# Performance work log

Hardware: AMD Instinct MI355X
Metric: run time of the kernel (lower is better)

Reference implementation:

```python
import jax, jax.numpy as jnp
import numpy as np

K = 16          # patch_size
P2 = 256        # patch_size**2
D_PD = 512      # learned base dictionary atoms (D_out_lam_pd)
D_LAM = 112     # adaptive atoms from sdict, = 8*14 (D_out_lam)
DD = D_PD + D_LAM  # 624
T = 5
INDICE = 112
MIN_V, MAX_V = 0.0, 1.0


def _idx(H, W, k, stride):
    oh = (H - k) // stride + 1
    ow = (W - k) // stride + 1
    r = jnp.arange(k)[:, None] + stride * jnp.arange(oh)[None, :]  # [k, oh]
    c = jnp.arange(k)[:, None] + stride * jnp.arange(ow)[None, :]  # [k, ow]
    return r[:, None, :, None], c[None, :, None, :], oh, ow


def _unfold(x, k, stride):
    # torch.nn.Unfold: [N, C*k*k, L] with (C, kh, kw) channel order, row-major L
    N, C, H, W = x.shape
    r, c, oh, ow = _idx(H, W, k, stride)
    return x[:, :, r, c].reshape(N, C * k * k, oh * ow)


def _fold(p, H, W, k):
    # torch.nn.functional.fold (col2im) with stride 1, overlap-add
    N, ckk, L = p.shape
    r, c, oh, ow = _idx(H, W, k, 1)
    C = ckk // (k * k)
    out = jnp.zeros((N, C, H, W), p.dtype)
    return out.at[:, :, r, c].add(p.reshape(N, C, k, k, oh, ow))


def _mlp(x, ws):
    # Linear + clamp(min=0) chain, no relu after last layer (dropout = eval identity)
    for w, b in ws[:-1]:
        x = jnp.maximum(x @ w + b, 0.0)
    w, b = ws[-1]
    return x @ w + b


def _cbam(x, w1, w2, conv_w):
    # standard CBAM: channel attention (shared MLP on avg+max pool) then 7x7 spatial attention
    def mlp(v):
        return jnp.maximum(v @ w1, 0.0) @ w2
    ca = jax.nn.sigmoid(mlp(x.mean(axis=(2, 3))) + mlp(x.max(axis=(2, 3))))
    x = x * ca[:, :, None, None]
    s = jnp.stack([x.mean(axis=1), x.max(axis=1)], axis=1)  # [N,2,h,w]
    sa = jax.lax.conv_general_dilated(s, conv_w, (1, 1), [(3, 3), (3, 3)],
                                      dimension_numbers=('NCHW', 'OIHW', 'NCHW'))
    return x * jax.nn.sigmoid(sa)


def _soft(x, l):
    return jnp.sign(x) * jnp.maximum(jnp.abs(x) - l, 0.0)


def _stage(img, Dict, c, sd_ws, ca1, ca2, saw, lam_ws, pd_ws, w_ws):
    N, C, H, W = img.shape
    uf = _unfold(img, K, 1).transpose(0, 2, 1)     # [N, L, 256]
    uf1 = _unfold(img, K, 8).transpose(0, 2, 1)    # [N, L1, 256]
    step = uf1.shape[1] // INDICE                  # static under jit
    ext = uf1[:, ::step, :][:, :INDICE, :]         # [N, 112, 256]
    sd = _mlp(ext, sd_ws)                          # linears1..4
    sd = sd / jnp.maximum(jnp.linalg.norm(sd, axis=-1, keepdims=True), 1e-12)
    sd = _cbam(sd.transpose(0, 2, 1).reshape(N, P2, 8, 14), ca1, ca2, saw)
    sd = sd.reshape(N, P2, INDICE)                 # [N, 256, 112]
    Dcat = jnp.concatenate([jnp.broadcast_to(Dict, (N,) + Dict.shape), sd], axis=-1)  # [N,256,624]
    # thresholds: l = cat(lpd, ls)
    thr = jnp.concatenate([_mlp(uf, pd_ws) / c, _mlp(uf, lam_ws) / c], axis=-1)  # [N,L,624]
    y = uf @ Dcat                                  # [N, L, 624]
    # S = (I - D^T D / c)^T; D^T D is symmetric so the transpose is a no-op
    S = jnp.eye(DD, dtype=img.dtype) - (Dcat.transpose(0, 2, 1) @ Dcat) / c
    z = _soft(y, thr)
    for _ in range(T):  # LISTA unrolled iterations (T static)
        z = _soft(z @ S + y / c, thr)
    Wg = jax.nn.sigmoid(_mlp(uf, w_ws))            # [N, L, 256]
    x_pred = jnp.clip(z @ Dcat.transpose(0, 2, 1), MIN_V, MAX_V) * Wg
    num = _fold(x_pred.transpose(0, 2, 1), H, W, K)
    den = _fold(Wg.transpose(0, 2, 1), H, W, K)    # fold of W * ones
    return num / den


def _forward(x, Dict, c, s1w, s1b, s2w, s2b, s3w, s3b, s4w, s4b, caw1, caw2, saw,
             a1w, a1b, a2w, a2b, a3w, a3b, p1w, p1b, p2w, p2b, p3w, p3b,
             b1w, b1b, b2w, b2b, b3w, b3b, q1w, q1b, q2w, q2b, q3w, q3b,
             w1w, w1b, w2w, w2b, w3w, w3b):
    sd_ws = [(s1w, s1b), (s2w, s2b), (s3w, s3b), (s4w, s4b)]
    w_ws = [(w1w, w1b), (w2w, w2b), (w3w, w3b)]
    res = _stage(x, Dict, c, sd_ws, caw1, caw2, saw,
                 [(a1w, a1b), (a2w, a2b), (a3w, a3b)],
                 [(p1w, p1b), (p2w, p2b), (p3w, p3b)], w_ws)
    res = _stage(res, Dict, c, sd_ws, caw1, caw2, saw,
                 [(b1w, b1b), (b2w, b2b), (b3w, b3b)],
                 [(q1w, q1b), (q2w, q2b), (q3w, q3b)], w_ws)
    return res


def setup_inputs() -> dict:
    key = jax.random.key(0)
    ks = iter(jax.random.split(key, 40))
    d = {}
    d['x'] = jax.random.uniform(next(ks), (2, 1, 128, 128), jnp.float32)
    Dm = jax.random.normal(next(ks), (P2, D_PD), jnp.float32)
    d['Dict'] = Dm / jnp.linalg.norm(Dm, axis=0, keepdims=True)  # unit-norm atoms
    d['c'] = jnp.asarray(10.0, jnp.float32)  # c > ||D^T D||_2
    dims = {'s1': (256, 512), 's2': (512, 1024), 's3': (1024, 512), 's4': (512, 256),
            'a1': (256, 1024), 'a2': (1024, 512), 'a3': (512, 112),
            'p1': (256, 1024), 'p2': (1024, 512), 'p3': (512, 512),
            'b1': (256, 1024), 'b2': (1024, 512), 'b3': (512, 112),
            'q1': (256, 1024), 'q2': (1024, 512), 'q3': (512, 512),
            'w1': (256, 1024), 'w2': (1024, 512), 'w3': (512, 256)}
    for name, (i, o) in dims.items():
        d[name + 'w'] = jax.random.normal(next(ks), (i, o), jnp.float32) / np.float32(np.sqrt(i))
        d[name + 'b'] = jnp.zeros((o,), jnp.float32)
    d['caw1'] = jax.random.normal(next(ks), (256, 512), jnp.float32) / np.float32(16.0)
    d['caw2'] = jax.random.normal(next(ks), (512, 256), jnp.float32) / np.float32(np.sqrt(512))
    d['saw'] = jax.random.normal(next(ks), (1, 2, 7, 7), jnp.float32) * np.float32(0.1)
    return d


def reference(x, Dict, c, s1w, s1b, s2w, s2b, s3w, s3b, s4w, s4b, caw1, caw2, saw,
              a1w, a1b, a2w, a2b, a3w, a3b, p1w, p1b, p2w, p2b, p3w, p3b,
              b1w, b1b, b2w, b2b, b3w, b3b, q1w, q1b, q2w, q2b, q3w, q3b,
              w1w, w1b, w2w, w2b, w3w, w3b):
    return _forward(x, Dict, c, s1w, s1b, s2w, s2b, s3w, s3b, s4w, s4b, caw1, caw2, saw,
                    a1w, a1b, a2w, a2b, a3w, a3b, p1w, p1b, p2w, p2b, p3w, p3b,
                    b1w, b1b, b2w, b2b, b3w, b3b, q1w, q1b, q2w, q2b, q3w, q3b,
                    w1w, w1b, w2w, w2b, w3w, w3b)
```

## Files before the change

### kernel.cpp

```cpp
#include <hip/hip_runtime.h>
#include <hip/hip_bf16.h>
#include <math.h>

#define L_LOC 12769
#define NB 2
#define NLR (NB * L_LOC)
#define NW 19

typedef short short8v __attribute__((ext_vector_type(8)));
typedef float f32x4 __attribute__((ext_vector_type(4)));
typedef __hip_bfloat16 bf16;

__device__ __forceinline__ float softf(float x, float l) {
  float a = fmaxf(fabsf(x) - l, 0.0f);
  return x > 0.0f ? a : (x < 0.0f ? -a : 0.0f);
}
__device__ __forceinline__ float sigf(float x) { return 1.0f / (1.0f + expf(-x)); }
__device__ __forceinline__ void split2(float v, bf16& h, bf16& l) {
  h = __float2bfloat16(v);
  l = __float2bfloat16(v - __bfloat162float(h));
}

enum { ME_RELU = 0, ME_SCALE = 1, ME_SIG = 2, ME_Y = 3, ME_SOFT = 4, ME_XP = 5,
       ME_SMAT = 6, ME_LIN = 7 };

template <int EPI, int TERMS, int WLO>
__global__ __launch_bounds__(256) void mgemm_k(
    const bf16* __restrict__ A, int lda, size_t aOff,
    const bf16* __restrict__ B0, const bf16* __restrict__ B1, int ldb, size_t bOff,
    void* __restrict__ Cv, int ldc, size_t cOff,
    bf16* __restrict__ Zp,
    const float* __restrict__ bias,
    const float* __restrict__ E1, const float* __restrict__ E2, int lde,
    const float* __restrict__ cptr, int bRow, int Rc, int r0, int N, int K)
{
  const int NPA = (TERMS >= 3) ? 2 : 1;
  const int NPB = (TERMS >= 2) ? 2 : 1;
  __shared__ char As[(TERMS >= 3) ? 2 : 1][8192];
  __shared__ char Bs[(TERMS >= 2) ? 2 : 1][8192];
  const int t = threadIdx.x;
  const int lane = t & 63, wv = t >> 6;
  const int wr = wv >> 1, wc = wv & 1;
  const int m0 = blockIdx.x * 128, n0 = blockIdx.y * 128;
  const int nb = (m0 >= bRow) ? 1 : 0;
  const bf16* __restrict__ Bt = nb ? B1 : B0;
  const int row16 = lane & 15, kg = lane >> 4;
  const int grow = t >> 2;
  const int gcol = (t & 3) * 8;
  f32x4 acc[4][4];
#pragma unroll
  for (int i = 0; i < 4; ++i)
#pragma unroll
    for (int j = 0; j < 4; ++j) { acc[i][j][0] = 0.f; acc[i][j][1] = 0.f; acc[i][j][2] = 0.f; acc[i][j][3] = 0.f; }

  for (int k0 = 0; k0 < K; k0 += 32) {
#pragma unroll
    for (int h = 0; h < NPA; ++h)
#pragma unroll
      for (int i = 0; i < 2; ++i) {
        const bf16* ga = A + h * aOff + (size_t)(m0 + i * 64 + grow) * lda + k0 + gcol;
        __builtin_amdgcn_global_load_lds(
            (const __attribute__((address_space(1))) void*)ga,
            (__attribute__((address_space(3))) void*)(As[h] + i * 4096 + wv * 1024), 16, 0, 0);
      }
#pragma unroll
    for (int h = 0; h < NPB; ++h)
#pragma unroll
      for (int i = 0; i < 2; ++i) {
        const bf16* gb = Bt + h * bOff + (size_t)(n0 + i * 64 + grow) * ldb + k0 + gcol;
        __builtin_amdgcn_global_load_lds(
            (const __attribute__((address_space(1))) void*)gb,
            (__attribute__((address_space(3))) void*)(Bs[h] + i * 4096 + wv * 1024), 16, 0, 0);
      }
    __syncthreads();
    short8v ah[4], al[4], bh[4], bl[4];
#pragma unroll
    for (int mi = 0; mi < 4; ++mi) {
      int o = (wr * 64 + mi * 16 + row16) * 64 + kg * 16;
      ah[mi] = *(const short8v*)(As[0] + o);
      if (TERMS >= 3) al[mi] = *(const short8v*)(As[NPA - 1] + o);
    }
#pragma unroll
    for (int ni = 0; ni < 4; ++ni) {
      int o = (wc * 64 + ni * 16 + row16) * 64 + kg * 16;
      bh[ni] = *(const short8v*)(Bs[0] + o);
      if (TERMS >= 2) bl[ni] = *(const short8v*)(Bs[NPB - 1] + o);
    }
#pragma unroll
    for (int mi = 0; mi < 4; ++mi)
#pragma unroll
      for (int ni = 0; ni < 4; ++ni) {
        if (TERMS >= 2)
          acc[mi][ni] = __builtin_amdgcn_mfma_f32_16x16x32_bf16(ah[mi], bl[ni], acc[mi][ni], 0, 0, 0);
        if (TERMS >= 3)
          acc[mi][ni] = __builtin_amdgcn_mfma_f32_16x16x32_bf16(al[mi], bh[ni], acc[mi][ni], 0, 0, 0);
        acc[mi][ni] = __builtin_amdgcn_mfma_f32_16x16x32_bf16(ah[mi], bh[ni], acc[mi][ni], 0, 0, 0);
      }
    __syncthreads();
  }

  float invc = 1.0f;
  if (EPI == ME_SCALE || EPI == ME_SOFT || EPI == ME_SMAT) invc = 1.0f / cptr[0];
  bf16* Cb = (bf16*)Cv;
  float* Cf = (float*)Cv;
#pragma unroll
  for (int ni = 0; ni < 4; ++ni) {
    int col = n0 + wc * 64 + ni * 16 + row16;
    const bool colok = col < N;
    float bv = 0.0f;
    if ((EPI == ME_RELU || EPI == ME_SCALE || EPI == ME_SIG || EPI == ME_LIN) && colok)
      bv = bias[col];
#pragma unroll
    for (int mi = 0; mi < 4; ++mi) {
      int rowb = m0 + wr * 64 + mi * 16 + kg * 4;
#pragma unroll
      for (int r = 0; r < 4; ++r) {
        int row = rowb + r;
        float v = acc[mi][ni][r];
        if (EPI == ME_RELU) {
          if (colok) {
            float o = fmaxf(v + bv, 0.0f);
            size_t ci = (size_t)row * ldc + col;
            if (WLO) {
              bf16 h, l; split2(o, h, l);
              Cb[ci] = h; Cb[ci + cOff] = l;
            } else {
              Cb[ci] = __float2bfloat16(o);
            }
          }
        } else if (EPI == ME_LIN) {
          if (colok && row < Rc) Cf[(size_t)row * ldc + col] = v + bv;
        } else if (EPI == ME_SCALE) {
          if (colok) Cf[(size_t)row * ldc + col] = (v + bv) * invc;
        } else if (EPI == ME_SIG) {
          if (colok) {
            int rl = row - nb * bRow;
            if (rl < Rc && rl >= 0)
              Cf[(size_t)col * NLR + (size_t)nb * L_LOC + r0 + rl] = sigf(v + bv);
          }
        } else if (EPI == ME_Y) {
          if (colok) {
            size_t e = (size_t)row * lde + col;
            Cf[(size_t)row * ldc + col] = v;
            Zp[(size_t)row * 640 + col] = __float2bfloat16(softf(v, E1[e]));
          }
        } else if (EPI == ME_SOFT) {
          if (colok) {
            size_t e = (size_t)row * lde + col;
            Cb[(size_t)row * ldc + col] = __float2bfloat16(softf(v + E1[e] * invc, E2[e]));
          }
        } else if (EPI == ME_XP) {
          int rl = row - nb * bRow;
          if (colok && rl < Rc && rl >= 0) {
            size_t g = (size_t)col * NLR + (size_t)nb * L_LOC + r0 + rl;
            Cf[g] = fminf(fmaxf(v, 0.0f), 1.0f) * E1[g];
          }
        } else {
          float o = (row < 624 && col < 624) ? ((row == col ? 1.0f : 0.0f) - v * invc) : 0.0f;
          bf16 h, l; split2(o, h, l);
          size_t ci = (size_t)row * ldc + col;
          Cb[ci] = h; Cb[ci + cOff] = l;
        }
      }
    }
  }
}

static void mgemm(hipStream_t st, int EPI, int terms, int wlo,
                  const bf16* A, int lda, size_t aOff,
                  const bf16* B0, const bf16* B1, int ldb, size_t bOff,
                  void* C, int ldc, size_t cOff,
                  bf16* Zp,
                  const float* bias, const float* E1, const float* E2, int lde,
                  const float* cptr, int bRow, int Rc, int r0,
                  int Mp, int N, int K)
{
  dim3 grid(Mp / 128, (N + 127) / 128), blk(256);
#define MG(ep, tm, wl) mgemm_k<ep, tm, wl><<<grid, blk, 0, st>>>(A, lda, aOff, B0, B1, ldb, bOff, C, ldc, cOff, Zp, bias, E1, E2, lde, cptr, bRow, Rc, r0, N, K)
  if (EPI == ME_RELU && terms == 1 && !wlo) { MG(ME_RELU, 1, 0); }
  else if (EPI == ME_RELU && terms == 1)    { MG(ME_RELU, 1, 1); }
  else if (EPI == ME_RELU)                  { MG(ME_RELU, 3, 1); }
  else if (EPI == ME_LIN)                   { MG(ME_LIN, 3, 0); }
  else if (EPI == ME_SCALE)                 { MG(ME_SCALE, 3, 0); }
  else if (EPI == ME_SIG)                   { MG(ME_SIG, 1, 0); }
  else if (EPI == ME_Y)                     { MG(ME_Y, 3, 0); }
  else if (EPI == ME_SOFT)                  { MG(ME_SOFT, 2, 0); }
  else if (EPI == ME_XP)                    { MG(ME_XP, 2, 0); }
  else                                      { MG(ME_SMAT, 3, 0); }
#undef MG
}

struct WTable {
  const float* src[NW];
  bf16* dst[NW];
  int K[NW], N[NW], Kp[NW], Np[NW];
  long long loOff[NW];
  int base[NW + 1];
};

__global__ void wtransall_k(WTable w) {
  int idx = blockIdx.x * 256 + threadIdx.x;
  if (idx >= w.base[NW]) return;
  int s = 0;
  while (s < NW - 1 && idx >= w.base[s + 1]) ++s;
  int li = idx - w.base[s];
  int Kp = w.Kp[s];
  int n = li / Kp, k = li - n * Kp;
  float v = (n < w.N[s] && k < w.K[s]) ? w.src[s][(size_t)k * w.N[s] + n] : 0.0f;
  bf16 h, l; split2(v, h, l);
  w.dst[s][li] = h;
  w.dst[s][li + w.loOff[s]] = l;
}

__global__ void extb_k(const float* __restrict__ img, bf16* __restrict__ dst) {
  int idx = blockIdx.x * 256 + threadIdx.x;
  int row = idx >> 8, p = idx & 255;
  float v = 0.0f;
  if (row < 224) {
    int n = row / 112, e = row - n * 112;
    int l1 = 2 * e, i1 = l1 / 15, j1 = l1 - i1 * 15;
    v = img[n * 16384 + (8 * i1 + (p >> 4)) * 128 + 8 * j1 + (p & 15)];
  }
  bf16 h, l; split2(v, h, l);
  dst[idx] = h; dst[idx + 65536] = l;
}

__global__ void rownorm224_k(float* sd) {
  int r = blockIdx.x, t = threadIdx.x;
  float v[4], s = 0.0f;
#pragma unroll
  for (int j = 0; j < 4; ++j) { v[j] = sd[r * 256 + t + 64 * j]; s += v[j] * v[j]; }
#pragma unroll
  for (int o = 1; o < 64; o <<= 1) s += __shfl_xor(s, o);
  float sc = 1.0f / fmaxf(sqrtf(s), 1e-12f);
#pragma unroll
  for (int j = 0; j < 4; ++j) sd[r * 256 + t + 64 * j] = v[j] * sc;
}

__global__ void meanmax_k(const float* __restrict__ sd, float* mv, float* xv) {
  int id = blockIdx.x * 256 + threadIdx.x;
  int n = id >> 8, ch = id & 255;
  float s = 0.0f, m = -INFINITY;
  for (int e = 0; e < 112; ++e) {
    float v = sd[(n * 112 + e) * 256 + ch];
    s += v; m = fmaxf(m, v);
  }
  mv[id] = s * (1.0f / 112.0f);
  xv[id] = m;
}

__global__ void cah_k(const float* __restrict__ mv, const float* __restrict__ xv,
                      const float* __restrict__ w1, float* hm, float* hx) {
  int id = blockIdx.x * 256 + threadIdx.x;
  int n = id >> 9, o = id & 511;
  float sm = 0.0f, sx = 0.0f;
#pragma unroll 4
  for (int i = 0; i < 256; ++i) {
    float w = w1[i * 512 + o];
    sm = fmaf(mv[n * 256 + i], w, sm);
    sx = fmaf(xv[n * 256 + i], w, sx);
  }
  hm[id] = fmaxf(sm, 0.0f);
  hx[id] = fmaxf(sx, 0.0f);
}

__global__ void cao_k(const float* __restrict__ hm, const float* __restrict__ hx,
                      const float* __restrict__ w2, float* ca) {
  int id = blockIdx.x * 256 + threadIdx.x;
  int n = id >> 8, ch = id & 255;
  float s = 0.0f;
#pragma unroll 4
  for (int o = 0; o < 512; ++o)
    s = fmaf(hm[n * 512 + o] + hx[n * 512 + o], w2[o * 256 + ch], s);
  ca[id] = sigf(s);
}

__global__ void spatial_k(const float* __restrict__ sd, const float* __restrict__ ca,
                          const float* __restrict__ saw, float* __restrict__ Dcat) {
  __shared__ float smean[112], smax[112];
  const int n = blockIdx.x, t = threadIdx.x;
  if (t < 112) {
    float sum = 0.0f, mx = -INFINITY;
    for (int ch = 0; ch < 256; ++ch) {
      float v = sd[(n * 112 + t) * 256 + ch] * ca[n * 256 + ch];
      Dcat[(size_t)n * 159744 + ch * 624 + 512 + t] = v;
      sum += v; mx = fmaxf(mx, v);
    }
    smean[t] = sum * (1.0f / 256.0f);
    smax[t] = mx;
  }
  __syncthreads();
  if (t < 112) {
    int h = t / 14, w = t % 14;
    float acc = 0.0f;
    for (int dh = 0; dh < 7; ++dh) {
      int hh = h + dh - 3; if (hh < 0 || hh >= 8) continue;
      for (int dw = 0; dw < 7; ++dw) {
        int ww = w + dw - 3; if (ww < 0 || ww >= 14) continue;
        int sp = hh * 14 + ww;
        acc += smean[sp] * saw[dh * 7 + dw] + smax[sp] * saw[49 + dh * 7 + dw];
      }
    }
    float sg = sigf(acc);
    for (int ch = 0; ch < 256; ++ch) Dcat[(size_t)n * 159744 + ch * 624 + 512 + t] *= sg;
  }
}

__global__ void dcatconv_k(const float* __restrict__ Dict, const float* __restrict__ Dc,
                           bf16* __restrict__ Db, bf16* __restrict__ DbT) {
  int idx = blockIdx.x * 256 + threadIdx.x;
  if (idx >= 327680) return;
  int n = idx / 163840, r = idx - n * 163840;
  int p = r / 640, a = r - p * 640;
  float v = 0.0f;
  if (a < 512)      v = Dict[p * 512 + a];
  else if (a < 624) v = Dc[(size_t)n * 159744 + p * 624 + a];
  bf16 h, l; split2(v, h, l);
  size_t base = (size_t)n * 327680;
  Db[base + p * 640 + a] = h;
  Db[base + 163840 + p * 640 + a] = l;
  DbT[base + (size_t)a * 256 + p] = h;
  DbT[base + 163840 + (size_t)a * 256 + p] = l;
}

__global__ void unfold_k(const float* __restrict__ img, bf16* __restrict__ uf,
                         int r0, int Rc, int bRowc, size_t pOff) {
  int bi = blockIdx.x;
  int nb = bi >= Rc;
  int rl = nb ? bi - Rc : bi;
  int row = nb * bRowc + rl;
  int p = threadIdx.x;
  int l = r0 + rl;
  int i0 = l / 113, j0 = l - i0 * 113;
  float v = img[nb * 16384 + (i0 + (p >> 4)) * 128 + j0 + (p & 15)];
  bf16 h, lo; split2(v, h, lo);
  size_t o = (size_t)row * 256 + p;
  uf[o] = h; uf[o + pOff] = lo;
}

__global__ void folddiv_k(const float* __restrict__ xpT, const float* __restrict__ wgT,
                          float* __restrict__ out) {
  int idx = blockIdx.x * 256 + threadIdx.x;
  if (idx >= 32768) return;
  int n = idx >> 14, rem = idx & 16383;
  int i = rem >> 7, j = rem & 127;
  float num = 0.0f, den = 0.0f;
  int kh0 = (i - 112 > 0) ? i - 112 : 0;
  int kh1 = (i < 15) ? i : 15;
  int kw0 = (j - 112 > 0) ? j - 112 : 0;
  int kw1 = (j < 15) ? j : 15;
  for (int kh = kh0; kh <= kh1; ++kh)
    for (int kw = kw0; kw <= kw1; ++kw) {
      int l = (i - kh) * 113 + (j - kw);
      size_t base = (size_t)(kh * 16 + kw) * NLR + (size_t)n * L_LOC + l;
      num += xpT[base];
      den += wgT[base];
    }
  out[idx] = num / den;
}

struct Bufs {
  float *xp, *wg, *Dcat_f, *sd, *res;
  float *mv, *xv, *hm, *hx, *ca;
  bf16 *Db, *DbT, *Sb;
  bf16 *extb, *sdh1, *sdh2, *sdh3;
  bf16 *uf, *h1, *h2, *z, *zn;
  float *thr, *y;
  size_t ufO, h2O;
  int R;
};

static void run_stage(hipStream_t st, const float* const* in, const float* img,
                      float* outimg, int pd0, int lam0,
                      bf16* const* WtPd, bf16* const* WtLam, bf16* const* WtW,
                      bf16* const* Ws, const Bufs& b)
{
  const float* cptr = in[2];
  const int BIG = 1 << 30;
  extb_k<<<dim3(256), dim3(256), 0, st>>>(img, b.extb);
  mgemm(st, ME_RELU, 3, 1, b.extb, 256, 65536, Ws[0], Ws[0], 256, 512 * 256,
        b.sdh1, 512, 256 * 512, 0, in[4], 0, 0, 0, cptr, BIG, 224, 0, 256, 512, 256);
  mgemm(st, ME_RELU, 3, 1, b.sdh1, 512, 256 * 512, Ws[1], Ws[1], 512, 1024 * 512,
        b.sdh2, 1024, 256 * 1024, 0, in[6], 0, 0, 0, cptr, BIG, 224, 0, 256, 1024, 512);
  mgemm(st, ME_RELU, 3, 1, b.sdh2, 1024, 256 * 1024, Ws[2], Ws[2], 1024, 512 * 1024,
        b.sdh3, 512, 256 * 512, 0, in[8], 0, 0, 0, cptr, BIG, 224, 0, 256, 512, 1024);
  mgemm(st, ME_LIN, 3, 0, b.sdh3, 512, 256 * 512, Ws[3], Ws[3], 512, 256 * 512,
        b.sd, 256, 0, 0, in[10], 0, 0, 0, cptr, BIG, 224, 0, 256, 256, 512);
  rownorm224_k<<<dim3(224), dim3(64), 0, st>>>(b.sd);
  meanmax_k<<<dim3(2), dim3(256), 0, st>>>(b.sd, b.mv, b.xv);
  cah_k<<<dim3(4), dim3(256), 0, st>>>(b.mv, b.xv, in[41], b.hm, b.hx);
  cao_k<<<dim3(2), dim3(256), 0, st>>>(b.hm, b.hx, in[42], b.ca);
  spatial_k<<<dim3(2), dim3(128), 0, st>>>(b.sd, b.ca, in[43], b.Dcat_f);
  dcatconv_k<<<dim3(1280), dim3(256), 0, st>>>(in[1], b.Dcat_f, b.Db, b.DbT);
  for (int n = 0; n < NB; ++n) {
    const bf16* Dt = b.DbT + (size_t)n * 327680;
    mgemm(st, ME_SMAT, 3, 0, Dt, 256, 163840, Dt, Dt, 256, 163840,
          b.Sb + (size_t)n * 819200, 640, 409600, 0,
          0, 0, 0, 0, cptr, BIG, 624, 0, 640, 640, 256);
  }

  for (int r0 = 0; r0 < L_LOC; r0 += b.R) {
    int Rc = L_LOC - r0; if (Rc > b.R) Rc = b.R;
    int bRowc = ((Rc + 127) / 128) * 128;
    int Mp = 2 * bRowc;
    unfold_k<<<dim3(2 * Rc), dim3(256), 0, st>>>(img, b.uf, r0, Rc, bRowc, b.ufO);
    mgemm(st, ME_RELU, 1, 0, b.uf, 256, b.ufO, WtPd[0], WtPd[0], 256, 1024 * 256,
          b.h1, 1024, 0, 0, in[pd0 + 1], 0, 0, 0, cptr, bRowc, Rc, r0, Mp, 1024, 256);
    mgemm(st, ME_RELU, 1, 1, b.h1, 1024, 0, WtPd[1], WtPd[1], 1024, 512 * 1024,
          b.h2, 512, b.h2O, 0, in[pd0 + 3], 0, 0, 0, cptr, bRowc, Rc, r0, Mp, 512, 1024);
    mgemm(st, ME_SCALE, 3, 0, b.h2, 512, b.h2O, WtPd[2], WtPd[2], 512, 512 * 512,
          b.thr, 640, 0, 0, in[pd0 + 5], 0, 0, 0, cptr, bRowc, Rc, r0, Mp, 512, 512);
    mgemm(st, ME_RELU, 1, 0, b.uf, 256, b.ufO, WtLam[0], WtLam[0], 256, 1024 * 256,
          b.h1, 1024, 0, 0, in[lam0 + 1], 0, 0, 0, cptr, bRowc, Rc, r0, Mp, 1024, 256);
    mgemm(st, ME_RELU, 1, 1, b.h1, 1024, 0, WtLam[1], WtLam[1], 1024, 512 * 1024,
          b.h2, 512, b.h2O, 0, in[lam0 + 3], 0, 0, 0, cptr, bRowc, Rc, r0, Mp, 512, 1024);
    mgemm(st, ME_SCALE, 3, 0, b.h2, 512, b.h2O, WtLam[2], WtLam[2], 512, 128 * 512,
          b.thr + 512, 640, 0, 0, in[lam0 + 5], 0, 0, 0, cptr, bRowc, Rc, r0, Mp, 112, 512);
    mgemm(st, ME_RELU, 1, 0, b.uf, 256, b.ufO, WtW[0], WtW[0], 256, 1024 * 256,
          b.h1, 1024, 0, 0, in[36], 0, 0, 0, cptr, bRowc, Rc, r0, Mp, 1024, 256);
    mgemm(st, ME_RELU, 1, 1, b.h1, 1024, 0, WtW[1], WtW[1], 1024, 512 * 1024,
          b.h2, 512, b.h2O, 0, in[38], 0, 0, 0, cptr, bRowc, Rc, r0, Mp, 512, 1024);
    mgemm(st, ME_SIG, 1, 0, b.h2, 512, b.h2O, WtW[2], WtW[2], 512, 256 * 512,
          b.wg, 0, 0, 0, in[40], 0, 0, 0, cptr, bRowc, Rc, r0, Mp, 256, 512);
    mgemm(st, ME_Y, 3, 0, b.uf, 256, b.ufO, b.DbT, b.DbT + 327680, 256, 163840,
          b.y, 640, 0, b.z, 0, b.thr, 0, 640, cptr, bRowc, Rc, r0, Mp, 624, 256);
    bf16* zi = b.z; bf16* zo = b.zn;
    for (int it = 0; it < 5; ++it) {
      mgemm(st, ME_SOFT, 2, 0, zi, 640, 0, b.Sb, b.Sb + 819200, 640, 409600,
            zo, 640, 0, 0, 0, b.y, b.thr, 640, cptr, bRowc, Rc, r0, Mp, 624, 640);
      bf16* tmp = zi; zi = zo; zo = tmp;
    }
    mgemm(st, ME_XP, 2, 0, zi, 640, 0, b.Db, b.Db + 327680, 640, 163840,
          b.xp, 0, 0, 0, 0, b.wg, 0, 0, cptr, bRowc, Rc, r0, Mp, 256, 640);
  }
  folddiv_k<<<dim3(128), dim3(256), 0, st>>>(b.xp, b.wg, outimg);
}

extern "C" void kernel_launch(void* const* d_in, const int* in_sizes, int n_in,
                              void* d_out, int out_size, void* d_ws, size_t ws_size,
                              hipStream_t stream)
{
  (void)in_sizes; (void)n_in; (void)out_size;
  const float* const* in = (const float* const*)d_in;
  char* base = (char*)d_ws;
  size_t off = 0;
  auto allocf = [&](size_t nelem) -> float* {
    float* p = (float*)(base + off);
    off += ((nelem * 4 + 255) / 256) * 256;
    return p;
  };
  auto allocb2 = [&](size_t nelem) -> bf16* {
    bf16* p = (bf16*)(base + off);
    off += ((nelem * 2 * 2 + 255) / 256) * 256;
    return p;
  };
  auto allocb1 = [&](size_t nelem) -> bf16* {
    bf16* p = (bf16*)(base + off);
    off += ((nelem * 2 + 255) / 256) * 256;
    return p;
  };
  Bufs b;
  b.xp = allocf((size_t)NLR * 256);
  b.wg = allocf((size_t)NLR * 256);
  b.Dcat_f = allocf(2 * 256 * 624);
  b.sd = allocf(224 * 256);
  b.res = allocf(2 * 16384);
  b.mv = allocf(512); b.xv = allocf(512);
  b.hm = allocf(1024); b.hx = allocf(1024);
  b.ca = allocf(512);
  b.Db = allocb2(2 * 163840);
  b.DbT = allocb2(2 * 163840);
  b.Sb = allocb2(2 * 409600);
  b.extb = allocb2(256 * 256);
  b.sdh1 = allocb2(256 * 512);
  b.sdh2 = allocb2(256 * 1024);
  b.sdh3 = allocb2(256 * 512);

  bf16 *Wa[3], *Wp[3], *Wb[3], *Wq[3], *Ww[3], *Ws[4];
  WTable wt;
  int ne = 0, tot = 0;
  auto addw = [&](const float* src, bf16* dst, int K, int N, int Kp, int Np) {
    wt.src[ne] = src; wt.dst[ne] = dst;
    wt.K[ne] = K; wt.N[ne] = N; wt.Kp[ne] = Kp; wt.Np[ne] = Np;
    wt.loOff[ne] = (long long)Np * Kp; wt.base[ne] = tot;
    tot += Np * Kp; ++ne;
  };
  int sdK[4] = {256, 512, 1024, 512}, sdN[4] = {512, 1024, 512, 256}, sdIdx[4] = {3, 5, 7, 9};
  for (int i = 0; i < 4; ++i) {
    Ws[i] = allocb2((size_t)sdN[i] * sdK[i]);
    addw(in[sdIdx[i]], Ws[i], sdK[i], sdN[i], sdK[i], sdN[i]);
  }
  struct WD { bf16** slot; int idx, K, N, Kp, Np; };
  WD wd[15] = {
    {&Wa[0], 11, 256, 1024, 256, 1024}, {&Wa[1], 13, 1024, 512, 1024, 512}, {&Wa[2], 15, 512, 112, 512, 128},
    {&Wp[0], 17, 256, 1024, 256, 1024}, {&Wp[1], 19, 1024, 512, 1024, 512}, {&Wp[2], 21, 512, 512, 512, 512},
    {&Wb[0], 23, 256, 1024, 256, 1024}, {&Wb[1], 25, 1024, 512, 1024, 512}, {&Wb[2], 27, 512, 112, 512, 128},
    {&Wq[0], 29, 256, 1024, 256, 1024}, {&Wq[1], 31, 1024, 512, 1024, 512}, {&Wq[2], 33, 512, 512, 512, 512},
    {&Ww[0], 35, 256, 1024, 256, 1024}, {&Ww[1], 37, 1024, 512, 1024, 512}, {&Ww[2], 39, 512, 256, 512, 256},
  };
  for (int i = 0; i < 15; ++i) {
    *wd[i].slot = allocb2((size_t)wd[i].Np * wd[i].Kp);
    addw(in[wd[i].idx], *wd[i].slot, wd[i].K, wd[i].N, wd[i].Kp, wd[i].Np);
  }
  wt.base[NW] = tot;
  wtransall_k<<<dim3((tot + 255) / 256), dim3(256), 0, stream>>>(wt);

  long long avail = (long long)ws_size - (long long)off - (1 << 20);
  long long perrow2 = 2LL * (12800 + 64);
  int R = 12800;
  if (avail / perrow2 < 12800) R = (int)(avail / perrow2);
  R &= ~127;
  if (R < 128) R = 128;
  b.R = R;
  size_t rows2 = (size_t)2 * R;
  b.uf = allocb2(rows2 * 256);  b.ufO = rows2 * 256;
  b.h1 = allocb1(rows2 * 1024);
  b.h2 = allocb2(rows2 * 512);  b.h2O = rows2 * 512;
  b.z = allocb1(rows2 * 640);
  b.zn = allocb1(rows2 * 640);
  b.thr = allocf(rows2 * 640);
  b.y = allocf(rows2 * 640);

  run_stage(stream, in, in[0], b.res, 17, 11, Wp, Wa, Ww, Ws, b);
  run_stage(stream, in, b.res, (float*)d_out, 29, 23, Wq, Wb, Ww, Ws, b);
}
```

Before: 3.189 ms.

## Store thresholds and y in bf16, swap GEMM grid order, parallelize spatial and fold kernels

The thr and y intermediates drop from fp32 to bf16 storage, which halves their traffic in the ME_Y and ME_SOFT epilogues that run every ISTA iteration. GEMM grid axes are swapped so consecutive blocks share the same row tile of A. spatial_k now uses wave-level shuffle reductions across 256 threads, and folddiv splits each pixel across 8 lanes with shuffle sums. The bf16 thresholds and y reduce precision in the soft-threshold recurrence, and the smaller per-row workspace allows larger row chunks.

```diff
diff --git a/kernel.cpp b/kernel.cpp
--- a/kernel.cpp
+++ b/kernel.cpp
@@ -31,7 +31,7 @@
     void* __restrict__ Cv, int ldc, size_t cOff,
     bf16* __restrict__ Zp,
     const float* __restrict__ bias,
-    const float* __restrict__ E1, const float* __restrict__ E2, int lde,
+    const void* __restrict__ E1, const void* __restrict__ E2, int lde,
     const float* __restrict__ cptr, int bRow, int Rc, int r0, int N, int K)
 {
   const int NPA = (TERMS >= 3) ? 2 : 1;
@@ -41,7 +41,7 @@
   const int t = threadIdx.x;
   const int lane = t & 63, wv = t >> 6;
   const int wr = wv >> 1, wc = wv & 1;
-  const int m0 = blockIdx.x * 128, n0 = blockIdx.y * 128;
+  const int m0 = blockIdx.y * 128, n0 = blockIdx.x * 128;
   const int nb = (m0 >= bRow) ? 1 : 0;
   const bf16* __restrict__ Bt = nb ? B1 : B0;
   const int row16 = lane & 15, kg = lane >> 4;
@@ -103,6 +103,9 @@
   if (EPI == ME_SCALE || EPI == ME_SOFT || EPI == ME_SMAT) invc = 1.0f / cptr[0];
   bf16* Cb = (bf16*)Cv;
   float* Cf = (float*)Cv;
+  const bf16* E1b = (const bf16*)E1;
+  const bf16* E2b = (const bf16*)E2;
+  const float* E1f = (const float*)E1;
 #pragma unroll
   for (int ni = 0; ni < 4; ++ni) {
     int col = n0 + wc * 64 + ni * 16 + row16;
@@ -131,7 +134,7 @@
         } else if (EPI == ME_LIN) {
           if (colok && row < Rc) Cf[(size_t)row * ldc + col] = v + bv;
         } else if (EPI == ME_SCALE) {
-          if (colok) Cf[(size_t)row * ldc + col] = (v + bv) * invc;
+          if (colok) Cb[(size_t)row * ldc + col] = __float2bfloat16((v + bv) * invc);
         } else if (EPI == ME_SIG) {
           if (colok) {
             int rl = row - nb * bRow;
@@ -141,19 +144,22 @@
         } else if (EPI == ME_Y) {
           if (colok) {
             size_t e = (size_t)row * lde + col;
-            Cf[(size_t)row * ldc + col] = v;
-            Zp[(size_t)row * 640 + col] = __float2bfloat16(softf(v, E1[e]));
+            Cb[(size_t)row * ldc + col] = __float2bfloat16(v);
+            float tv = __bfloat162float(E1b[e]);
+            Zp[(size_t)row * 640 + col] = __float2bfloat16(softf(v, tv));
           }
         } else if (EPI == ME_SOFT) {
           if (colok) {
             size_t e = (size_t)row * lde + col;
-            Cb[(size_t)row * ldc + col] = __float2bfloat16(softf(v + E1[e] * invc, E2[e]));
+            float yv = __bfloat162float(E1b[e]);
+            float tv = __bfloat162float(E2b[e]);
+            Cb[(size_t)row * ldc + col] = __float2bfloat16(softf(v + yv * invc, tv));
           }
         } else if (EPI == ME_XP) {
           int rl = row - nb * bRow;
           if (colok && rl < Rc && rl >= 0) {
             size_t g = (size_t)col * NLR + (size_t)nb * L_LOC + r0 + rl;
-            Cf[g] = fminf(fmaxf(v, 0.0f), 1.0f) * E1[g];
+            Cf[g] = fminf(fmaxf(v, 0.0f), 1.0f) * E1f[g];
           }
         } else {
           float o = (row < 624 && col < 624) ? ((row == col ? 1.0f : 0.0f) - v * invc) : 0.0f;
@@ -171,11 +177,11 @@
                   const bf16* B0, const bf16* B1, int ldb, size_t bOff,
                   void* C, int ldc, size_t cOff,
                   bf16* Zp,
-                  const float* bias, const float* E1, const float* E2, int lde,
+                  const float* bias, const void* E1, const void* E2, int lde,
                   const float* cptr, int bRow, int Rc, int r0,
                   int Mp, int N, int K)
 {
-  dim3 grid(Mp / 128, (N + 127) / 128), blk(256);
+  dim3 grid((N + 127) / 128, Mp / 128), blk(256);
 #define MG(ep, tm, wl) mgemm_k<ep, tm, wl><<<grid, blk, 0, st>>>(A, lda, aOff, B0, B1, ldb, bOff, C, ldc, cOff, Zp, bias, E1, E2, lde, cptr, bRow, Rc, r0, N, K)
   if (EPI == ME_RELU && terms == 1 && !wlo) { MG(ME_RELU, 1, 0); }
   else if (EPI == ME_RELU && terms == 1)    { MG(ME_RELU, 1, 1); }
@@ -275,34 +281,54 @@
   ca[id] = sigf(s);
 }
 
-__global__ void spatial_k(const float* __restrict__ sd, const float* __restrict__ ca,
-                          const float* __restrict__ saw, float* __restrict__ Dcat) {
-  __shared__ float smean[112], smax[112];
-  const int n = blockIdx.x, t = threadIdx.x;
-  if (t < 112) {
+__global__ __launch_bounds__(256) void spatial_k(
+    const float* __restrict__ sd, const float* __restrict__ ca,
+    const float* __restrict__ saw, float* __restrict__ Dcat)
+{
+  __shared__ float smean[112], smax[112], sa[112];
+  const int n = blockIdx.x;
+  const int t = threadIdx.x, lane = t & 63, w = t >> 6;
+  float cav[4];
+#pragma unroll
+  for (int c = 0; c < 4; ++c) cav[c] = ca[n * 256 + lane + 64 * c];
+  for (int s = w * 28; s < w * 28 + 28; ++s) {
     float sum = 0.0f, mx = -INFINITY;
-    for (int ch = 0; ch < 256; ++ch) {
-      float v = sd[(n * 112 + t) * 256 + ch] * ca[n * 256 + ch];
-      Dcat[(size_t)n * 159744 + ch * 624 + 512 + t] = v;
+#pragma unroll
+    for (int c = 0; c < 4; ++c) {
+      int ch = lane + 64 * c;
+      float v = sd[(n * 112 + s) * 256 + ch] * cav[c];
+      Dcat[(size_t)n * 159744 + ch * 624 + 512 + s] = v;
       sum += v; mx = fmaxf(mx, v);
     }
-    smean[t] = sum * (1.0f / 256.0f);
-    smax[t] = mx;
+#pragma unroll
+    for (int o = 1; o < 64; o <<= 1) {
+      sum += __shfl_xor(sum, o);
+      mx = fmaxf(mx, __shfl_xor(mx, o));
+    }
+    if (lane == 0) { smean[s] = sum * (1.0f / 256.0f); smax[s] = mx; }
   }
   __syncthreads();
   if (t < 112) {
-    int h = t / 14, w = t % 14;
+    int h = t / 14, wd = t % 14;
     float acc = 0.0f;
     for (int dh = 0; dh < 7; ++dh) {
       int hh = h + dh - 3; if (hh < 0 || hh >= 8) continue;
       for (int dw = 0; dw < 7; ++dw) {
-        int ww = w + dw - 3; if (ww < 0 || ww >= 14) continue;
+        int ww = wd + dw - 3; if (ww < 0 || ww >= 14) continue;
         int sp = hh * 14 + ww;
         acc += smean[sp] * saw[dh * 7 + dw] + smax[sp] * saw[49 + dh * 7 + dw];
       }
     }
-    float sg = sigf(acc);
-    for (int ch = 0; ch < 256; ++ch) Dcat[(size_t)n * 159744 + ch * 624 + 512 + t] *= sg;
+    sa[t] = sigf(acc);
+  }
+  __syncthreads();
+  for (int s = w * 28; s < w * 28 + 28; ++s) {
+    float sg = sa[s];
+#pragma unroll
+    for (int c = 0; c < 4; ++c) {
+      int ch = lane + 64 * c;
+      Dcat[(size_t)n * 159744 + ch * 624 + 512 + s] *= sg;
+    }
   }
 }
 
@@ -341,22 +367,29 @@
 __global__ void folddiv_k(const float* __restrict__ xpT, const float* __restrict__ wgT,
                           float* __restrict__ out) {
   int idx = blockIdx.x * 256 + threadIdx.x;
-  if (idx >= 32768) return;
-  int n = idx >> 14, rem = idx & 16383;
+  if (idx >= 262144) return;
+  int g = idx & 7;
+  int pix = idx >> 3;
+  int n = pix >> 14, rem = pix & 16383;
   int i = rem >> 7, j = rem & 127;
   float num = 0.0f, den = 0.0f;
   int kh0 = (i - 112 > 0) ? i - 112 : 0;
   int kh1 = (i < 15) ? i : 15;
   int kw0 = (j - 112 > 0) ? j - 112 : 0;
   int kw1 = (j < 15) ? j : 15;
-  for (int kh = kh0; kh <= kh1; ++kh)
+  for (int kh = kh0 + ((g - kh0) & 7); kh <= kh1; kh += 8)
     for (int kw = kw0; kw <= kw1; ++kw) {
       int l = (i - kh) * 113 + (j - kw);
       size_t base = (size_t)(kh * 16 + kw) * NLR + (size_t)n * L_LOC + l;
       num += xpT[base];
       den += wgT[base];
     }
-  out[idx] = num / den;
+#pragma unroll
+  for (int o = 1; o < 8; o <<= 1) {
+    num += __shfl_xor(num, o);
+    den += __shfl_xor(den, o);
+  }
+  if (g == 0) out[pix] = num / den;
 }
 
 struct Bufs {
@@ -364,8 +397,7 @@
   float *mv, *xv, *hm, *hx, *ca;
   bf16 *Db, *DbT, *Sb;
   bf16 *extb, *sdh1, *sdh2, *sdh3;
-  bf16 *uf, *h1, *h2, *z, *zn;
-  float *thr, *y;
+  bf16 *uf, *h1, *h2, *z, *zn, *thr, *y;
   size_t ufO, h2O;
   int R;
 };
@@ -390,7 +422,7 @@
   meanmax_k<<<dim3(2), dim3(256), 0, st>>>(b.sd, b.mv, b.xv);
   cah_k<<<dim3(4), dim3(256), 0, st>>>(b.mv, b.xv, in[41], b.hm, b.hx);
   cao_k<<<dim3(2), dim3(256), 0, st>>>(b.hm, b.hx, in[42], b.ca);
-  spatial_k<<<dim3(2), dim3(128), 0, st>>>(b.sd, b.ca, in[43], b.Dcat_f);
+  spatial_k<<<dim3(2), dim3(256), 0, st>>>(b.sd, b.ca, in[43], b.Dcat_f);
   dcatconv_k<<<dim3(1280), dim3(256), 0, st>>>(in[1], b.Dcat_f, b.Db, b.DbT);
   for (int n = 0; n < NB; ++n) {
     const bf16* Dt = b.DbT + (size_t)n * 327680;
@@ -433,7 +465,7 @@
     mgemm(st, ME_XP, 2, 0, zi, 640, 0, b.Db, b.Db + 327680, 640, 163840,
           b.xp, 0, 0, 0, 0, b.wg, 0, 0, cptr, bRowc, Rc, r0, Mp, 256, 640);
   }
-  folddiv_k<<<dim3(128), dim3(256), 0, st>>>(b.xp, b.wg, outimg);
+  folddiv_k<<<dim3(1024), dim3(256), 0, st>>>(b.xp, b.wg, outimg);
 }
 
 extern "C" void kernel_launch(void* const* d_in, const int* in_sizes, int n_in,
@@ -506,7 +538,7 @@
   wtransall_k<<<dim3((tot + 255) / 256), dim3(256), 0, stream>>>(wt);
 
   long long avail = (long long)ws_size - (long long)off - (1 << 20);
-  long long perrow2 = 2LL * (12800 + 64);
+  long long perrow2 = 2LL * (10240 + 64);
   int R = 12800;
   if (avail / perrow2 < 12800) R = (int)(avail / perrow2);
   R &= ~127;
@@ -518,8 +550,8 @@
   b.h2 = allocb2(rows2 * 512);  b.h2O = rows2 * 512;
   b.z = allocb1(rows2 * 640);
   b.zn = allocb1(rows2 * 640);
-  b.thr = allocf(rows2 * 640);
-  b.y = allocf(rows2 * 640);
+  b.thr = allocb1(rows2 * 640);
+  b.y = allocb1(rows2 * 640);
 
   run_stage(stream, in, in[0], b.res, 17, 11, Wp, Wa, Ww, Ws, b);
   run_stage(stream, in, b.res, (float*)d_out, 29, 23, Wq, Wb, Ww, Ws, b);
```

Result: no change. 3.134 ms (-1.7%).
